# Performance work log

Measured on AMD Instinct MI355X. Metric: run time of the kernel, lower is better.

## Reference

```python
import jax, jax.numpy as jnp
import numpy as np

TEMPERATURE = 0.1
NORMALIZE = True


def setup_inputs() -> dict:
    key = jax.random.key(0)
    k1, k2 = jax.random.split(key)
    B, D = 4096, 512
    return {
        "z_i": jax.random.normal(k1, (B, D), dtype=jnp.float32),
        "z_j": jax.random.normal(k2, (B, D), dtype=jnp.float32),
    }


def _l2norm(x):
    return x / jnp.sqrt(jnp.sum(x * x, axis=-1, keepdims=True))


def reference(z_i, z_j):
    if NORMALIZE:
        z_i = _l2norm(z_i)
        z_j = _l2norm(z_j)
    B = z_i.shape[0]

    inv_t = 1.0 / TEMPERATURE
    logits_aa = (z_i @ z_i.T) * inv_t  # [B, B]
    logits_bb = (z_j @ z_j.T) * inv_t
    logits_ab = (z_i @ z_j.T) * inv_t
    logits_ba = (z_j @ z_i.T) * inv_t

    # Static off-diagonal column indices: row i keeps cols 0..B-1 except i,
    # in ascending order (matches torch boolean-mask row-major extraction).
    j = jnp.arange(B - 1)[None, :]
    i = jnp.arange(B)[:, None]
    idx = j + (j >= i)  # [B, B-1] int32

    take = lambda m: jnp.take_along_axis(m, idx, axis=1)  # [B, B-1]

    pos = jnp.concatenate([jnp.diagonal(logits_ab), jnp.diagonal(logits_ba)])[:, None]  # [2B, 1]
    neg_a = jnp.concatenate([take(logits_aa), take(logits_ab)], axis=1)  # [B, 2(B-1)]
    neg_b = jnp.concatenate([take(logits_ba), take(logits_bb)], axis=1)
    neg = jnp.concatenate([neg_a, neg_b], axis=0)  # [2B, 2(B-1)]

    logits = jnp.concatenate([pos, neg], axis=1)  # [2B, 2B-1]
    logp = jax.nn.log_softmax(logits, axis=1)
    # Original forward uses labels = torch.ones(2B).long() -> target class 1.
    loss = -jnp.mean(logp[:, 1])
    return loss
```

## Files before the change

kernel.cpp:

```cpp
#include <hip/hip_runtime.h>
#include <hip/hip_bf16.h>
#include <hip/hip_fp8.h>


#define BB 4096
#define DD 512
#define NN 8192
#define TILE 128
#define NPAN 64
#define NBLK 2080

typedef __attribute__((ext_vector_type(4)))  float f32x4;
typedef __attribute__((ext_vector_type(16))) float f32x16;
typedef __attribute__((ext_vector_type(4)))  int   i32x4;
typedef __attribute__((ext_vector_type(8)))  int   i32x8;

#define AS1 __attribute__((address_space(1)))
#define AS3 __attribute__((address_space(3)))
static __device__ __forceinline__ void gload_lds16(const void* g, void* l) {
    __builtin_amdgcn_global_load_lds((const AS1 void*)g, (AS3 void*)l, 16, 0, 0);
}

__global__ __launch_bounds__(256)
void normalize_kernel(const float* __restrict__ zi, const float* __restrict__ zj,
                      unsigned char* __restrict__ M, float* __restrict__ wacc) {
    const int wave = threadIdx.x >> 6;
    const int lane = threadIdx.x & 63;
    const int row  = blockIdx.x * 4 + wave;
    if (blockIdx.x == 0 && threadIdx.x == 0) wacc[0] = 0.f;
    const float* src = (row < BB) ? (zi + (size_t)row * DD)
                                  : (zj + (size_t)(row - BB) * DD);
    float4 v0 = ((const float4*)src)[lane * 2 + 0];
    float4 v1 = ((const float4*)src)[lane * 2 + 1];
    float ss = v0.x*v0.x + v0.y*v0.y + v0.z*v0.z + v0.w*v0.w
             + v1.x*v1.x + v1.y*v1.y + v1.z*v1.z + v1.w*v1.w;
    #pragma unroll
    for (int off = 1; off <= 32; off <<= 1) ss += __shfl_xor(ss, off);
    const float inv = rsqrtf(ss);
    const float vals[8] = {v0.x*inv, v0.y*inv, v0.z*inv, v0.w*inv,
                           v1.x*inv, v1.y*inv, v1.z*inv, v1.w*inv};
    union { long u; unsigned char b[8]; } pk;
    #pragma unroll
    for (int j = 0; j < 8; ++j)
        pk.b[j] = __hip_cvt_float_to_fp8(vals[j], __HIP_SATFINITE, __HIP_E4M3);
    ((long*)(M + (size_t)row * DD))[lane] = pk.u;
}

__global__ __launch_bounds__(256, 2)
void gram_lse_kernel(const unsigned char* __restrict__ Mg,
                     float* __restrict__ rpart, float* __restrict__ targets) {
    __shared__ __align__(16) char Bs[TILE * DD];

    const int d = blockIdx.x;
    const int p = (d & 7) * 260 + (d >> 3);
    int by = (int)((sqrtf(8.0f * (float)p + 1.0f) - 1.0f) * 0.5f);
    while ((by + 1) * (by + 2) / 2 <= p) ++by;
    while (by * (by + 1) / 2 > p) --by;
    const int bx = p - by * (by + 1) / 2;

    const int rowBase = bx * TILE;
    const int colBase = by * TILE;
    const bool diag = (bx == by);
    const int tid  = threadIdx.x;
    const int wave = tid >> 6;
    const int lane = tid & 63;
    const int l31 = lane & 31;
    const int h0  = lane >> 5;

    #pragma unroll
    for (int i = 0; i < 16; ++i) {
        const int row = i * 8 + (tid >> 5);
        const int sg  = (tid & 31) ^ (row & 31);
        gload_lds16(Mg + (size_t)(colBase + row) * DD + sg * 16,
                    Bs + ((size_t)i * 256 + tid) * 16);
    }

    const unsigned char* Arow =
        Mg + (size_t)(rowBase + wave * 32 + l31) * DD + h0 * 32;

    __syncthreads();

    f32x16 acc[4] = {};
    const int rb0 = l31 * DD;
    i32x4 c0a = *(const i32x4*)(Arow +   0), c0b = *(const i32x4*)(Arow +  16);
    i32x4 c1a = *(const i32x4*)(Arow +  64), c1b = *(const i32x4*)(Arow +  80);
    #pragma unroll
    for (int t = 0; t < 8; ++t) {
        const i32x8 a = __builtin_shufflevector(c0a, c0b, 0, 1, 2, 3, 4, 5, 6, 7);
        c0a = c1a; c0b = c1b;
        if (t + 2 < 8) {
            c1a = *(const i32x4*)(Arow + (t + 2) * 64);
            c1b = *(const i32x4*)(Arow + (t + 2) * 64 + 16);
        }
        const int g0 = t * 4 + h0 * 2;
        const int p0 = (g0 ^ l31) * 16;
        const int p1 = ((g0 ^ 1) ^ l31) * 16;
        #pragma unroll
        for (int ni = 0; ni < 4; ++ni) {
            const char* rbase = Bs + rb0 + ni * 32 * DD;
            i32x4 lo = *(const i32x4*)(rbase + p0);
            i32x4 hi = *(const i32x4*)(rbase + p1);
            i32x8 b = __builtin_shufflevector(lo, hi, 0, 1, 2, 3, 4, 5, 6, 7);
            acc[ni] = __builtin_amdgcn_mfma_scale_f32_32x32x64_f8f6f4(
                a, b, acc[ni], 0, 0, 0, 0x7F7F7F7F, 0, 0x7F7F7F7F);
        }
    }

    const float C10 = 14.42695040888963f;
    float rs[16] = {};
    float cs[4]  = {};
    #pragma unroll
    for (int ni = 0; ni < 4; ++ni) {
        const int gcol = colBase + ni * 32 + l31;
        #pragma unroll
        for (int r = 0; r < 16; ++r) {
            const int lrow = (r & 3) + 8 * (r >> 2) + 4 * h0;
            const int grow = rowBase + wave * 32 + lrow;
            float e = __builtin_amdgcn_exp2f(fmaf(acc[ni][r], C10, -C10));
            if (grow == gcol) e = 0.f;
            rs[r] += e;
            cs[ni] += e;
            if (rowBase == 0 && grow < 2) {
                const int j0 = ((gcol & (BB - 1)) == 0) ? 1 : 0;
                if (grow == j0) targets[gcol] = 10.f * acc[ni][r];
            }
        }
    }
    #pragma unroll
    for (int m = 1; m <= 16; m <<= 1)
        #pragma unroll
        for (int r = 0; r < 16; ++r)
            rs[r] += __shfl_xor(rs[r], m);
    if (l31 == 0) {
        #pragma unroll
        for (int r = 0; r < 16; ++r)
            rpart[(size_t)by * NN + rowBase + wave * 32
                  + (r & 3) + 8 * (r >> 2) + 4 * h0] = rs[r];
    }
    if (!diag) {
        #pragma unroll
        for (int ni = 0; ni < 4; ++ni)
            cs[ni] += __shfl_xor(cs[ni], 32);
        float* cpart = (float*)Bs;
        __syncthreads();
        if (h0 == 0) {
            #pragma unroll
            for (int ni = 0; ni < 4; ++ni)
                cpart[wave * TILE + ni * 32 + l31] = cs[ni];
        }
        __syncthreads();
        if (tid < TILE) {
            float v = cpart[tid] + cpart[TILE + tid]
                    + cpart[2 * TILE + tid] + cpart[3 * TILE + tid];
            rpart[(size_t)bx * NN + colBase + tid] = v;
        }
    }
}

__global__ __launch_bounds__(256)
void reduce_kernel(const float* __restrict__ rpart,
                   const float* __restrict__ targets, float* __restrict__ wacc) {
    const int i = blockIdx.x * 256 + threadIdx.x;
    float s = 0.f;
    #pragma unroll 8
    for (int sl = 0; sl < NPAN; ++sl)
        s += rpart[(size_t)sl * NN + i];
    float term = targets[i] - 10.f - __logf(s);
    #pragma unroll
    for (int off = 1; off <= 32; off <<= 1) term += __shfl_xor(term, off);
    __shared__ float red[4];
    if ((threadIdx.x & 63) == 0) red[threadIdx.x >> 6] = term;
    __syncthreads();
    if (threadIdx.x == 0)
        atomicAdd(wacc, red[0] + red[1] + red[2] + red[3]);
}

__global__ void write_kernel(const float* __restrict__ wacc,
                             float* __restrict__ out) {
    out[0] = -wacc[0] / (float)NN;
}

extern "C" void kernel_launch(void* const* d_in, const int* in_sizes, int n_in,
                              void* d_out, int out_size, void* d_ws, size_t ws_size,
                              hipStream_t stream) {
    const float* zi = (const float*)d_in[0];
    const float* zj = (const float*)d_in[1];

    unsigned char* M = (unsigned char*)d_ws;
    float* rpart   = (float*)((char*)d_ws + (size_t)NN * DD);
    float* targets = rpart + (size_t)NPAN * NN;
    float* wacc    = targets + NN;
    float* out = (float*)d_out;

    normalize_kernel<<<NN / 4, 256, 0, stream>>>(zi, zj, M, wacc);
    gram_lse_kernel<<<NBLK, 256, 0, stream>>>(M, rpart, targets);
    reduce_kernel<<<NN / 256, 256, 0, stream>>>(rpart, targets, wacc);
    write_kernel<<<1, 1, 0, stream>>>(wacc, out);
}
```

Baseline: 107.2 us.

## Retile Gram kernel to 256x64 tiles with per-wave column partials and higher occupancy

Changes the symmetric Gram tiling from 128x128 square tiles to 256x64 rectangular tiles with a new triangular index mapping. LDS per block shrinks to 32KB so occupancy rises to 4 blocks per CU, and each wave now computes a 64x64 sub-block. Column sums are written per wave into extra rpart slices instead of being combined through LDS with two barriers. The partial-sum buffer grows to 256 slices, which the normalize kernel zeroes and the reduce kernel reads, adding memory traffic. The A operand is also reloaded from global memory without the previous software prefetch.

```diff
diff --git a/kernel.cpp b/kernel.cpp
--- a/kernel.cpp
+++ b/kernel.cpp
@@ -6,9 +6,12 @@
 #define BB 4096
 #define DD 512
 #define NN 8192
-#define TILE 128
-#define NPAN 64
-#define NBLK 2080
+#define TM 256
+#define TN 64
+#define NRP 32
+#define NCT 128
+#define NBLK 2112
+#define NSLICE 256
 
 typedef __attribute__((ext_vector_type(4)))  float f32x4;
 typedef __attribute__((ext_vector_type(16))) float f32x16;
@@ -23,11 +26,15 @@
 
 __global__ __launch_bounds__(256)
 void normalize_kernel(const float* __restrict__ zi, const float* __restrict__ zj,
-                      unsigned char* __restrict__ M, float* __restrict__ wacc) {
+                      unsigned char* __restrict__ M, float* __restrict__ rpart,
+                      float* __restrict__ wacc) {
+    const int gt = blockIdx.x * 256 + threadIdx.x;
+    ((f32x4*)rpart)[gt] = (f32x4){0.f, 0.f, 0.f, 0.f};
+    if (gt == 0) wacc[0] = 0.f;
+
     const int wave = threadIdx.x >> 6;
     const int lane = threadIdx.x & 63;
     const int row  = blockIdx.x * 4 + wave;
-    if (blockIdx.x == 0 && threadIdx.x == 0) wacc[0] = 0.f;
     const float* src = (row < BB) ? (zi + (size_t)row * DD)
                                   : (zj + (size_t)(row - BB) * DD);
     float4 v0 = ((const float4*)src)[lane * 2 + 0];
@@ -46,21 +53,21 @@
     ((long*)(M + (size_t)row * DD))[lane] = pk.u;
 }
 
-__global__ __launch_bounds__(256, 2)
+__global__ __launch_bounds__(256, 4)
 void gram_lse_kernel(const unsigned char* __restrict__ Mg,
                      float* __restrict__ rpart, float* __restrict__ targets) {
-    __shared__ __align__(16) char Bs[TILE * DD];
+    __shared__ __align__(16) char Bs[TN * DD];
 
     const int d = blockIdx.x;
-    const int p = (d & 7) * 260 + (d >> 3);
-    int by = (int)((sqrtf(8.0f * (float)p + 1.0f) - 1.0f) * 0.5f);
-    while ((by + 1) * (by + 2) / 2 <= p) ++by;
-    while (by * (by + 1) / 2 > p) --by;
-    const int bx = p - by * (by + 1) / 2;
-
-    const int rowBase = bx * TILE;
-    const int colBase = by * TILE;
-    const bool diag = (bx == by);
+    const int p = (d & 7) * (NBLK / 8) + (d >> 3);
+    int bx = (int)((130.f - sqrtf(16900.f - 8.f * (float)p)) * 0.25f);
+    while (130 * (bx + 1) - 2 * (bx + 1) * (bx + 1) <= p) ++bx;
+    while (130 * bx - 2 * bx * bx > p) --bx;
+    const int cy = 4 * bx + (p - (130 * bx - 2 * bx * bx));
+    const bool inDiag = (cy - 4 * bx) < 4;
+
+    const int rowBase = bx * TM;
+    const int colBase = cy * TN;
     const int tid  = threadIdx.x;
     const int wave = tid >> 6;
     const int lane = tid & 63;
@@ -68,91 +75,87 @@
     const int h0  = lane >> 5;
 
     #pragma unroll
-    for (int i = 0; i < 16; ++i) {
+    for (int i = 0; i < 8; ++i) {
         const int row = i * 8 + (tid >> 5);
-        const int sg  = (tid & 31) ^ (row & 31);
-        gload_lds16(Mg + (size_t)(colBase + row) * DD + sg * 16,
+        const int sgr = (tid & 31) ^ (row & 31);
+        gload_lds16(Mg + (size_t)(colBase + row) * DD + sgr * 16,
                     Bs + ((size_t)i * 256 + tid) * 16);
     }
 
-    const unsigned char* Arow =
-        Mg + (size_t)(rowBase + wave * 32 + l31) * DD + h0 * 32;
+    const unsigned char* A0 =
+        Mg + (size_t)(rowBase + wave * 64 + l31) * DD + h0 * 32;
 
     __syncthreads();
 
-    f32x16 acc[4] = {};
-    const int rb0 = l31 * DD;
-    i32x4 c0a = *(const i32x4*)(Arow +   0), c0b = *(const i32x4*)(Arow +  16);
-    i32x4 c1a = *(const i32x4*)(Arow +  64), c1b = *(const i32x4*)(Arow +  80);
+    f32x16 acc[2][2] = {};
+    const char* Brow0 = Bs + l31 * DD;
     #pragma unroll
     for (int t = 0; t < 8; ++t) {
-        const i32x8 a = __builtin_shufflevector(c0a, c0b, 0, 1, 2, 3, 4, 5, 6, 7);
-        c0a = c1a; c0b = c1b;
-        if (t + 2 < 8) {
-            c1a = *(const i32x4*)(Arow + (t + 2) * 64);
-            c1b = *(const i32x4*)(Arow + (t + 2) * 64 + 16);
+        i32x4 a0l = *(const i32x4*)(A0 + t * 64);
+        i32x4 a0h = *(const i32x4*)(A0 + t * 64 + 16);
+        i32x4 a1l = *(const i32x4*)(A0 + 32 * DD + t * 64);
+        i32x4 a1h = *(const i32x4*)(A0 + 32 * DD + t * 64 + 16);
+        const i32x8 a0 = __builtin_shufflevector(a0l, a0h, 0, 1, 2, 3, 4, 5, 6, 7);
+        const i32x8 a1 = __builtin_shufflevector(a1l, a1h, 0, 1, 2, 3, 4, 5, 6, 7);
+        const int p0 = ((t * 4 + h0 * 2) ^ l31) * 16;
+        #pragma unroll
+        for (int ni = 0; ni < 2; ++ni) {
+            const char* rb = Brow0 + ni * 32 * DD;
+            i32x4 lo = *(const i32x4*)(rb + p0);
+            i32x4 hi = *(const i32x4*)(rb + (p0 ^ 16));
+            i32x8 b = __builtin_shufflevector(lo, hi, 0, 1, 2, 3, 4, 5, 6, 7);
+            acc[0][ni] = __builtin_amdgcn_mfma_scale_f32_32x32x64_f8f6f4(
+                a0, b, acc[0][ni], 0, 0, 0, 0x7F7F7F7F, 0, 0x7F7F7F7F);
+            acc[1][ni] = __builtin_amdgcn_mfma_scale_f32_32x32x64_f8f6f4(
+                a1, b, acc[1][ni], 0, 0, 0, 0x7F7F7F7F, 0, 0x7F7F7F7F);
         }
-        const int g0 = t * 4 + h0 * 2;
-        const int p0 = (g0 ^ l31) * 16;
-        const int p1 = ((g0 ^ 1) ^ l31) * 16;
-        #pragma unroll
-        for (int ni = 0; ni < 4; ++ni) {
-            const char* rbase = Bs + rb0 + ni * 32 * DD;
-            i32x4 lo = *(const i32x4*)(rbase + p0);
-            i32x4 hi = *(const i32x4*)(rbase + p1);
-            i32x8 b = __builtin_shufflevector(lo, hi, 0, 1, 2, 3, 4, 5, 6, 7);
-            acc[ni] = __builtin_amdgcn_mfma_scale_f32_32x32x64_f8f6f4(
-                a, b, acc[ni], 0, 0, 0, 0x7F7F7F7F, 0, 0x7F7F7F7F);
-        }
     }
 
     const float C10 = 14.42695040888963f;
-    float rs[16] = {};
-    float cs[4]  = {};
-    #pragma unroll
-    for (int ni = 0; ni < 4; ++ni) {
+    float rs[2][16] = {};
+    float cs[2] = {0.f, 0.f};
+    #pragma unroll
+    for (int ni = 0; ni < 2; ++ni) {
         const int gcol = colBase + ni * 32 + l31;
         #pragma unroll
-        for (int r = 0; r < 16; ++r) {
-            const int lrow = (r & 3) + 8 * (r >> 2) + 4 * h0;
-            const int grow = rowBase + wave * 32 + lrow;
-            float e = __builtin_amdgcn_exp2f(fmaf(acc[ni][r], C10, -C10));
-            if (grow == gcol) e = 0.f;
-            rs[r] += e;
-            cs[ni] += e;
-            if (rowBase == 0 && grow < 2) {
-                const int j0 = ((gcol & (BB - 1)) == 0) ? 1 : 0;
-                if (grow == j0) targets[gcol] = 10.f * acc[ni][r];
+        for (int mi = 0; mi < 2; ++mi) {
+            #pragma unroll
+            for (int r = 0; r < 16; ++r) {
+                const int lrow = (r & 3) + 8 * (r >> 2) + 4 * h0;
+                const int grow = rowBase + wave * 64 + mi * 32 + lrow;
+                float e = __builtin_amdgcn_exp2f(fmaf(acc[mi][ni][r], C10, -C10));
+                if (inDiag && grow == gcol) e = 0.f;
+                rs[mi][r] += e;
+                cs[ni] += e;
+                if (rowBase == 0 && wave == 0 && mi == 0 && grow < 2) {
+                    const int j0 = ((gcol & (BB - 1)) == 0) ? 1 : 0;
+                    if (grow == j0) targets[gcol] = 10.f * acc[mi][ni][r];
+                }
             }
         }
     }
     #pragma unroll
     for (int m = 1; m <= 16; m <<= 1)
         #pragma unroll
-        for (int r = 0; r < 16; ++r)
-            rs[r] += __shfl_xor(rs[r], m);
+        for (int mi = 0; mi < 2; ++mi)
+            #pragma unroll
+            for (int r = 0; r < 16; ++r)
+                rs[mi][r] += __shfl_xor(rs[mi][r], m);
     if (l31 == 0) {
         #pragma unroll
-        for (int r = 0; r < 16; ++r)
-            rpart[(size_t)by * NN + rowBase + wave * 32
-                  + (r & 3) + 8 * (r >> 2) + 4 * h0] = rs[r];
-    }
-    if (!diag) {
-        #pragma unroll
-        for (int ni = 0; ni < 4; ++ni)
-            cs[ni] += __shfl_xor(cs[ni], 32);
-        float* cpart = (float*)Bs;
-        __syncthreads();
+        for (int mi = 0; mi < 2; ++mi)
+            #pragma unroll
+            for (int r = 0; r < 16; ++r)
+                rpart[(size_t)cy * NN + rowBase + wave * 64 + mi * 32
+                      + (r & 3) + 8 * (r >> 2) + 4 * h0] = rs[mi][r];
+    }
+    if (!inDiag) {
+        cs[0] += __shfl_xor(cs[0], 32);
+        cs[1] += __shfl_xor(cs[1], 32);
         if (h0 == 0) {
-            #pragma unroll
-            for (int ni = 0; ni < 4; ++ni)
-                cpart[wave * TILE + ni * 32 + l31] = cs[ni];
-        }
-        __syncthreads();
-        if (tid < TILE) {
-            float v = cpart[tid] + cpart[TILE + tid]
-                    + cpart[2 * TILE + tid] + cpart[3 * TILE + tid];
-            rpart[(size_t)bx * NN + colBase + tid] = v;
+            const size_t sbase = (size_t)(NCT + bx * 4 + wave) * NN + colBase;
+            rpart[sbase + l31]      = cs[0];
+            rpart[sbase + 32 + l31] = cs[1];
         }
     }
 }
@@ -163,7 +166,7 @@
     const int i = blockIdx.x * 256 + threadIdx.x;
     float s = 0.f;
     #pragma unroll 8
-    for (int sl = 0; sl < NPAN; ++sl)
+    for (int sl = 0; sl < NSLICE; ++sl)
         s += rpart[(size_t)sl * NN + i];
     float term = targets[i] - 10.f - __logf(s);
     #pragma unroll
@@ -188,11 +191,11 @@
 
     unsigned char* M = (unsigned char*)d_ws;
     float* rpart   = (float*)((char*)d_ws + (size_t)NN * DD);
-    float* targets = rpart + (size_t)NPAN * NN;
+    float* targets = rpart + (size_t)NSLICE * NN;
     float* wacc    = targets + NN;
     float* out = (float*)d_out;
 
-    normalize_kernel<<<NN / 4, 256, 0, stream>>>(zi, zj, M, wacc);
+    normalize_kernel<<<NN / 4, 256, 0, stream>>>(zi, zj, M, rpart, wacc);
     gram_lse_kernel<<<NBLK, 256, 0, stream>>>(M, rpart, targets);
     reduce_kernel<<<NN / 256, 256, 0, stream>>>(rpart, targets, wacc);
     write_kernel<<<1, 1, 0, stream>>>(wacc, out);
```

Result: slower. 129.4 us (+20.7%).
